# Kernel tuning notes

Hardware: AMD Instinct MI355X
Metric: run time of the kernel (lower is better)

## Reference

```python
import jax, jax.numpy as jnp
import numpy as np
from jax import lax

NL, HID, DIN, DST, DCONV, DTR = 4, 256, 512, 16, 4, 16  # layers, d_model, expand*d_model, d_state, d_conv, dt_rank
B, H, W = 4, 256, 256


def setup_inputs() -> dict:
    key = jax.random.key(0)
    ks = jax.random.split(key, 8)
    def n(k, s, sc=0.02):
        return jax.random.normal(k, s, dtype=jnp.float32) * sc
    return {
        "x": jax.random.normal(ks[0], (B, 3, H, W), dtype=jnp.float32),
        "conv1_w": n(ks[1], (HID // 2, 3, 3, 3), 0.1), "conv1_b": jnp.zeros((HID // 2,), jnp.float32),
        "gn1_w": jnp.ones((HID // 2,), jnp.float32), "gn1_b": jnp.zeros((HID // 2,), jnp.float32),
        "conv2_w": n(ks[2], (HID, HID // 2, 3, 3), 0.05), "conv2_b": jnp.zeros((HID,), jnp.float32),
        "gn2_w": jnp.ones((HID,), jnp.float32), "gn2_b": jnp.zeros((HID,), jnp.float32),
        "ln_w": jnp.ones((NL, HID), jnp.float32), "ln_b": jnp.zeros((NL, HID), jnp.float32),
        "in_proj_w": n(ks[3], (NL, 2 * DIN, HID)),
        "conv1d_w": n(ks[4], (NL, DIN, 1, DCONV), 0.1), "conv1d_b": jnp.zeros((NL, DIN), jnp.float32),
        "x_proj_w": n(ks[5], (NL, DTR + 2 * DST, DIN)),
        "dt_proj_w": n(ks[6], (NL, DIN, DTR), 0.1),
        "dt_proj_b": jnp.full((NL, DIN), -4.6, dtype=jnp.float32),  # softplus(-4.6) ~ 0.01
        "A_log": jnp.broadcast_to(jnp.log(jnp.arange(1, DST + 1, dtype=jnp.float32)), (NL, DIN, DST)) + jnp.zeros((NL, DIN, DST), jnp.float32),
        "D": jnp.ones((NL, DIN), jnp.float32),
        "out_proj_w": n(ks[7], (NL, HID, DIN)),
    }


def conv2d_s2(x, w, b):
    y = lax.conv_general_dilated(x, w, (2, 2), [(1, 1), (1, 1)],
                                 dimension_numbers=('NCHW', 'OIHW', 'NCHW'))
    return y + b[None, :, None, None]


def group_norm(x, w, b, groups=8, eps=1e-5):
    Bb, C, Hh, Ww = x.shape
    xg = x.reshape(Bb, groups, C // groups, Hh, Ww)
    m = xg.mean((2, 3, 4), keepdims=True)
    v = xg.var((2, 3, 4), keepdims=True)
    xg = (xg - m) * lax.rsqrt(v + eps)
    return xg.reshape(Bb, C, Hh, Ww) * w[None, :, None, None] + b[None, :, None, None]


def layer_norm(x, w, b, eps=1e-5):
    m = x.mean(-1, keepdims=True)
    v = x.var(-1, keepdims=True)
    return (x - m) * lax.rsqrt(v + eps) * w + b


def mamba(x, ipw, cw, cb, xpw, dpw, dpb, A_log, Dp, opw):
    # x: [B, L, HID]
    Bb, L, _ = x.shape
    xz = jnp.einsum('bld,ed->ble', x, ipw)           # [B, L, 2*DIN]
    xc, z = jnp.split(xz, 2, axis=-1)
    # depthwise causal conv1d over L
    u = xc.transpose(0, 2, 1)                        # [B, DIN, L]
    u = lax.conv_general_dilated(u, cw, (1,), [(DCONV - 1, 0)],
                                 dimension_numbers=('NCH', 'OIH', 'NCH'),
                                 feature_group_count=DIN)
    xc = jax.nn.silu(u + cb[None, :, None]).transpose(0, 2, 1)  # [B, L, DIN]
    x_dbl = jnp.einsum('bld,ed->ble', xc, xpw)       # [B, L, DTR+2*DST]
    dt, Bm, Cm = jnp.split(x_dbl, [DTR, DTR + DST], axis=-1)
    delta = jax.nn.softplus(jnp.einsum('blr,dr->bld', dt, dpw) + dpb)  # [B, L, DIN]
    A = -jnp.exp(A_log)                              # [DIN, DST]
    dA = jnp.exp(jnp.einsum('bld,dn->bldn', delta, A))
    dBu = jnp.einsum('bld,bln,bld->bldn', delta, Bm, xc)

    def step(h, inp):
        dA_t, dBu_t, C_t = inp
        h = dA_t * h + dBu_t                         # [B, DIN, DST]
        return h, jnp.einsum('bdn,bn->bd', h, C_t)

    h0 = jnp.zeros((Bb, DIN, DST), x.dtype)
    _, ys = lax.scan(step, h0, (dA.transpose(1, 0, 2, 3), dBu.transpose(1, 0, 2, 3), Cm.transpose(1, 0, 2)))
    y = ys.transpose(1, 0, 2) + xc * Dp              # [B, L, DIN]
    y = y * jax.nn.silu(z)
    return jnp.einsum('bld,ed->ble', y, opw)         # [B, L, HID]


def reference(x, conv1_w, conv1_b, gn1_w, gn1_b, conv2_w, conv2_b, gn2_w, gn2_b,
              ln_w, ln_b, in_proj_w, conv1d_w, conv1d_b, x_proj_w, dt_proj_w,
              dt_proj_b, A_log, D, out_proj_w):
    y = jax.nn.silu(group_norm(conv2d_s2(x, conv1_w, conv1_b), gn1_w, gn1_b))
    y = jax.nn.silu(group_norm(conv2d_s2(y, conv2_w, conv2_b), gn2_w, gn2_b))
    Bb, C, h, w = y.shape
    s = y.reshape(Bb, C, h * w).transpose(0, 2, 1)   # b (h w) c
    for i in range(NL):
        s = s + mamba(layer_norm(s, ln_w[i], ln_b[i]), in_proj_w[i], conv1d_w[i],
                      conv1d_b[i], x_proj_w[i], dt_proj_w[i], dt_proj_b[i],
                      A_log[i], D[i], out_proj_w[i])
    return (s, h, w)
```

## Files before the change

### kernel.cpp

```cpp
#include <hip/hip_runtime.h>
#include <math.h>

#define BB 4
#define C1 128
#define H1 128
#define W1 128
#define C2 256
#define H2 64
#define W2 64
#define LSEQ 4096
#define HID 256
#define DIN 512
#define DST 16
#define DTR 16
#define NL 4
#define NCHUNK 64
#define LCH 64

typedef unsigned short u16;
using short8 = __attribute__((ext_vector_type(8))) short;
using f32x4  = __attribute__((ext_vector_type(4))) float;
using f32x2  = __attribute__((ext_vector_type(2))) float;

static __device__ __forceinline__ float dsilu(float x){
    return x / (1.0f + __expf(-x));
}
static __device__ __forceinline__ u16 f2bf(float f){
    unsigned u = __float_as_uint(f);
    u += 0x7FFF + ((u >> 16) & 1);
    return (u16)(u >> 16);
}
static __device__ __forceinline__ float bf2f(u16 v){
    return __uint_as_float(((unsigned)v) << 16);
}

#define GLL16(g, l) __builtin_amdgcn_global_load_lds( \
    (const __attribute__((address_space(1))) void*)(g), \
    (__attribute__((address_space(3))) void*)(l), 16, 0, 0)
#define GLL4(g, l) __builtin_amdgcn_global_load_lds( \
    (const __attribute__((address_space(1))) void*)(g), \
    (__attribute__((address_space(3))) void*)(l), 4, 0, 0)

#define VMW(n) asm volatile("s_waitcnt vmcnt(" #n ")" ::: "memory")

static __device__ __forceinline__ void blockbar(){
    asm volatile("" ::: "memory");
    __builtin_amdgcn_s_barrier();
    asm volatile("" ::: "memory");
}

__global__ void f2bf_kernel(const float* __restrict__ src, u16* __restrict__ dst){
    int idx = blockIdx.x * 256 + threadIdx.x;
    dst[idx] = f2bf(src[idx]);
}
__global__ void wdt_prep_kernel(const float* __restrict__ xpw, const float* __restrict__ dpw,
                                u16* __restrict__ wcomb){
    int idx = blockIdx.x * 256 + threadIdx.x;
    int k = idx & 511;
    int n = (idx >> 9) % 640;
    int layer = idx / (640*512);
    u16 val = 0;
    if(n < 512){
        const float* dp = dpw + ((long)layer*512 + n)*16;
        const float* xp = xpw + (long)layer*48*512 + k;
        float acc = 0.f;
        #pragma unroll
        for(int r = 0; r < 16; ++r) acc = fmaf(dp[r], xp[(long)r*512], acc);
        val = f2bf(acc);
    } else if(n < 544){
        int row = n - 512 + 16;
        val = f2bf(xpw[((long)layer*48 + row)*512 + k]);
    }
    wcomb[((long)layer*640 + n)*512 + k] = val;
}
__global__ void c2w_prep_kernel(const float* __restrict__ src, u16* __restrict__ dst){
    int idx = blockIdx.x * 256 + threadIdx.x;
    int ci = idx & 127, p = (idx >> 7) % 9, co = idx / (9*128);
    int kh = p / 3, kw = p - 3*kh;
    dst[idx] = f2bf(src[((co*128 + ci)*3 + kh)*3 + kw]);
}
__global__ void xt_border_kernel(unsigned* __restrict__ xt){
    int idx = blockIdx.x * 256 + threadIdx.x;
    int c2 = idx & 63;
    int cell = (idx >> 6) % 516;
    int b = idx / (516*64);
    int ih, iw;
    if(cell < 130){ ih = 0; iw = cell; }
    else if(cell < 260){ ih = 129; iw = cell - 130; }
    else if(cell < 388){ iw = 0; ih = cell - 259; }
    else { iw = 129; ih = cell - 387; }
    xt[((long)(b*130 + ih)*130 + iw)*64 + c2] = 0;
}

__global__ __launch_bounds__(256) void conv1_kernel(
        const float* __restrict__ x, const float* __restrict__ w,
        const float* __restrict__ bias, float* __restrict__ y){
    __shared__ float xs[9][260];
    int oh = blockIdx.x, b = blockIdx.y;
    int tid = threadIdx.x;
    #pragma unroll
    for(int r = 0; r < 9; ++r){
        int ci = r / 3, kh = r - 3*ci;
        int ih = 2*oh - 1 + kh;
        float v = 0.f;
        if(ih >= 0) v = x[((b*3 + ci)*256 + ih)*256 + tid];
        xs[r][tid + 1] = v;
        if(tid == 0) xs[r][0] = 0.f;
    }
    __syncthreads();
    int co = tid >> 1, h = tid & 1;
    float wr[27];
    #pragma unroll
    for(int j = 0; j < 27; ++j) wr[j] = w[co*27 + j];
    float bz = bias[co];
    long obase = ((long)((b*128 + co)*128 + oh))*128 + h*64;
    #pragma unroll 4
    for(int i = 0; i < 64; ++i){
        int iw0 = 2*(h*64 + i);
        float acc = bz;
        #pragma unroll
        for(int r = 0; r < 9; ++r){
            acc = fmaf(xs[r][iw0+0], wr[r*3+0], acc);
            acc = fmaf(xs[r][iw0+1], wr[r*3+1], acc);
            acc = fmaf(xs[r][iw0+2], wr[r*3+2], acc);
        }
        y[obase + i] = acc;
    }
}

__global__ void zero_stats_kernel(float* __restrict__ stats){
    stats[threadIdx.x] = 0.0f;
}

__global__ void gn_stats_kernel(const float* __restrict__ x, float* __restrict__ stats,
                                int elems_per_group){
    const int EPB = 16384;
    long base = (long)blockIdx.x * EPB;
    int g = (int)(base / elems_per_group);
    float s = 0.f, ss = 0.f;
    for(int j = threadIdx.x; j < EPB; j += 256){
        float v = x[base + j];
        s += v; ss += v*v;
    }
    #pragma unroll
    for(int off = 32; off; off >>= 1){
        s  += __shfl_down(s,  off);
        ss += __shfl_down(ss, off);
    }
    __shared__ float ls[4], lss[4];
    int wid = threadIdx.x >> 6, lane = threadIdx.x & 63;
    if(lane == 0){ ls[wid] = s; lss[wid] = ss; }
    __syncthreads();
    if(threadIdx.x == 0){
        atomicAdd(&stats[g],      ls[0]+ls[1]+ls[2]+ls[3]);
        atomicAdd(&stats[32+g], lss[0]+lss[1]+lss[2]+lss[3]);
    }
}

__global__ void gn1_transform_kernel(const float* __restrict__ y1, const float* __restrict__ stats,
                                     const float* __restrict__ w, const float* __restrict__ bias,
                                     u16* __restrict__ xt){
    __shared__ float tile[32][33];
    int b = blockIdx.z >> 7, ih = blockIdx.z & 127;
    int c0 = blockIdx.y * 32, w0 = blockIdx.x * 32;
    int tx = threadIdx.x, ty = threadIdx.y;
    const float cnt = 16.f * 128.f * 128.f;
    #pragma unroll
    for(int i = 0; i < 4; ++i){
        int ci = c0 + ty + i*8;
        int g = b*8 + (ci >> 4);
        float mean = stats[g] / cnt;
        float var  = stats[32+g] / cnt - mean*mean;
        float rstd = rsqrtf(var + 1e-5f);
        float v = y1[(((long)(b*C1 + ci))*H1 + ih)*W1 + w0 + tx];
        tile[ty + i*8][tx] = dsilu((v - mean) * rstd * w[ci] + bias[ci]);
    }
    __syncthreads();
    #pragma unroll
    for(int i = 0; i < 4; ++i){
        int iwl = ty + i*8;
        xt[((long)(b*130 + ih + 1)*130 + (w0 + iwl + 1))*128 + c0 + tx] = f2bf(tile[tx][iwl]);
    }
}

__global__ __launch_bounds__(256) void conv2gemm_bf16_kernel(
        const u16* __restrict__ xt, const u16* __restrict__ w2,
        const float* __restrict__ bias, float* __restrict__ y2t){
    __shared__ u16 Asm[3][64*32];
    __shared__ u16 Bsm[3][128*32];
    int m0 = blockIdx.x * 64, n0 = blockIdx.y * 128;
    int tid = threadIdx.x;
    long abase;
    {
        int r = tid >> 2;
        int kq = ((tid & 3) ^ ((r >> 1) & 3)) * 8;
        int m = m0 + r;
        int b = m >> 12, oh = (m >> 6) & 63, ow = m & 63;
        abase = ((long)(b*130 + 2*oh)*130 + 2*ow)*128 + kq;
    }
    int lda = tid*8;
    const u16* bbase[2]; int ldb[2];
    #pragma unroll
    for(int it = 0; it < 2; ++it){
        int c = it*256 + tid;
        int r = c >> 2;
        int kq = ((c & 3) ^ ((r >> 1) & 3)) * 8;
        bbase[it] = w2 + (long)(n0 + r)*1152 + kq;
        ldb[it] = c*8;
    }
    int wave = tid >> 6, lane = tid & 63;
    int wr = wave >> 1, wc = wave & 1;
    int lm = lane & 15, lq = lane >> 4;
    int swq = (lq ^ ((lm >> 1) & 3)) * 8;
    f32x4 acc[2][4] = {};
    #pragma unroll
    for(int pt = 0; pt < 2; ++pt){
        int p = pt >> 2, cs = pt & 3;
        int kh = p / 3, kw = p - 3*kh;
        int ao = (kh*130 + kw)*128 + cs*32;
        GLL16(xt + abase + ao, &Asm[pt][lda]);
        #pragma unroll
        for(int it = 0; it < 2; ++it)
            GLL16(bbase[it] + pt*32, &Bsm[pt][ldb[it]]);
    }
    for(int kk = 0; kk < 36; ++kk){
        int cur = kk % 3;
        if(kk + 2 < 36){
            int k2 = kk + 2;
            int nxt = (kk + 2) % 3;
            int p = k2 >> 2, cs = k2 & 3;
            int kh = p / 3, kw = p - 3*kh;
            int ao = (kh*130 + kw)*128 + cs*32;
            GLL16(xt + abase + ao, &Asm[nxt][lda]);
            #pragma unroll
            for(int it = 0; it < 2; ++it)
                GLL16(bbase[it] + k2*32, &Bsm[nxt][ldb[it]]);
            VMW(6);
        } else if(kk + 1 < 36){
            VMW(3);
        } else {
            VMW(0);
        }
        blockbar();
        short8 af[2], bf[4];
        #pragma unroll
        for(int i = 0; i < 2; ++i)
            af[i] = *(const short8*)&Asm[cur][(wr*32 + i*16 + lm)*32 + swq];
        #pragma unroll
        for(int j = 0; j < 4; ++j)
            bf[j] = *(const short8*)&Bsm[cur][(wc*64 + j*16 + lm)*32 + swq];
        #pragma unroll
        for(int i = 0; i < 2; ++i)
            #pragma unroll
            for(int j = 0; j < 4; ++j)
                acc[i][j] = __builtin_amdgcn_mfma_f32_16x16x32_bf16(af[i], bf[j], acc[i][j], 0, 0, 0);
        __builtin_amdgcn_sched_barrier(0);
        blockbar();
    }
    #pragma unroll
    for(int i = 0; i < 2; ++i){
        long row = m0 + wr*32 + i*16 + lq*4;
        #pragma unroll
        for(int j = 0; j < 4; ++j){
            int col = n0 + wc*64 + j*16 + lm;
            float bz = bias[col];
            #pragma unroll
            for(int r = 0; r < 4; ++r)
                y2t[(row + r)*256L + col] = acc[i][j][r] + bz;
        }
    }
}

__global__ void gn2t_stats_kernel(const float* __restrict__ y2t, float* __restrict__ stats){
    int b = blockIdx.y;
    long row0 = (long)b*LSEQ + blockIdx.x*64;
    int c = threadIdx.x;
    float s = 0.f, ss = 0.f;
    for(int r = 0; r < 64; ++r){
        float v = y2t[(row0 + r)*C2 + c];
        s += v; ss += v*v;
    }
    #pragma unroll
    for(int off = 16; off; off >>= 1){
        s  += __shfl_down(s,  off);
        ss += __shfl_down(ss, off);
    }
    if((c & 31) == 0){
        int g = b*8 + (c >> 5);
        atomicAdd(&stats[g], s);
        atomicAdd(&stats[32+g], ss);
    }
}

__global__ void gn2t_apply_ln_kernel(const float* __restrict__ y2t, const float* __restrict__ stats,
                                     const float* __restrict__ gw, const float* __restrict__ gb,
                                     const float* __restrict__ lw, const float* __restrict__ lb,
                                     float* __restrict__ s, u16* __restrict__ xln){
    long row = blockIdx.x;
    int c = threadIdx.x;
    int b = (int)(row >> 12);
    int g = b*8 + (c >> 5);
    const float cnt = 32.f * (float)LSEQ;
    float mean = stats[g] / cnt;
    float var  = stats[32+g] / cnt - mean*mean;
    float rstd = rsqrtf(var + 1e-5f);
    float v = dsilu((y2t[row*HID + c] - mean) * rstd * gw[c] + gb[c]);
    s[row*HID + c] = v;
    float sm = v, sq = v*v;
    #pragma unroll
    for(int off = 32; off; off >>= 1){
        sm += __shfl_down(sm, off);
        sq += __shfl_down(sq, off);
    }
    __shared__ float pa[4], pb[4], res[2];
    int wid = c >> 6, lane = c & 63;
    if(lane == 0){ pa[wid] = sm; pb[wid] = sq; }
    __syncthreads();
    if(c == 0){
        float t  = pa[0]+pa[1]+pa[2]+pa[3];
        float tt = pb[0]+pb[1]+pb[2]+pb[3];
        float m2 = t / 256.f;
        float v2 = tt / 256.f - m2*m2;
        res[0] = m2; res[1] = rsqrtf(v2 + 1e-5f);
    }
    __syncthreads();
    xln[row*HID + c] = f2bf((v - res[0]) * res[1] * lw[c] + lb[c]);
}

__global__ __launch_bounds__(256) void gemm_bf16_kernel(
        const u16* __restrict__ A, const u16* __restrict__ B, void* __restrict__ Cv,
        int K, int Nact, int ldc, int mode){
    __shared__ u16 Asm[3][128*32];
    __shared__ u16 Bsm[3][128*32];
    int m0 = blockIdx.x * 128, n0 = blockIdx.y * 128;
    int tid = threadIdx.x;
    int wave = tid >> 6, lane = tid & 63;
    int wr = wave >> 1, wc = wave & 1;
    int lm = lane & 15, lq = lane >> 4;
    int swq = (lq ^ ((lm >> 1) & 3)) * 8;
    const u16* ag[2]; const u16* bg[2]; int ldst[2];
    #pragma unroll
    for(int it = 0; it < 2; ++it){
        int c = it*256 + tid;
        int r = c >> 2;
        int kq = ((c & 3) ^ ((r >> 1) & 3)) * 8;
        ag[it] = A + (long)(m0 + r)*K + kq;
        bg[it] = B + (long)(n0 + r)*K + kq;
        ldst[it] = c*8;
    }
    f32x4 acc[4][4] = {};
    int nk = K >> 5;
    #pragma unroll
    for(int pt = 0; pt < 2; ++pt){
        int ko = pt << 5;
        #pragma unroll
        for(int it = 0; it < 2; ++it){
            GLL16(ag[it] + ko, &Asm[pt][ldst[it]]);
            GLL16(bg[it] + ko, &Bsm[pt][ldst[it]]);
        }
    }
    for(int kt = 0; kt < nk; ++kt){
        int cur = kt % 3;
        if(kt + 2 < nk){
            int nxt = (kt + 2) % 3;
            int ko = (kt + 2) << 5;
            #pragma unroll
            for(int it = 0; it < 2; ++it){
                GLL16(ag[it] + ko, &Asm[nxt][ldst[it]]);
                GLL16(bg[it] + ko, &Bsm[nxt][ldst[it]]);
            }
            VMW(8);
        } else if(kt + 1 < nk){
            VMW(4);
        } else {
            VMW(0);
        }
        blockbar();
        short8 af[4], bf[4];
        #pragma unroll
        for(int i = 0; i < 4; ++i){
            af[i] = *(const short8*)&Asm[cur][(wr*64 + i*16 + lm)*32 + swq];
            bf[i] = *(const short8*)&Bsm[cur][(wc*64 + i*16 + lm)*32 + swq];
        }
        #pragma unroll
        for(int i = 0; i < 4; ++i)
            #pragma unroll
            for(int j = 0; j < 4; ++j)
                acc[i][j] = __builtin_amdgcn_mfma_f32_16x16x32_bf16(af[i], bf[j], acc[i][j], 0, 0, 0);
        __builtin_amdgcn_sched_barrier(0);
        blockbar();
    }
    #pragma unroll
    for(int i = 0; i < 4; ++i){
        long row = m0 + wr*64 + i*16 + lq*4;
        #pragma unroll
        for(int j = 0; j < 4; ++j){
            int col = n0 + wc*64 + j*16 + lm;
            if(col < Nact){
                #pragma unroll
                for(int r = 0; r < 4; ++r){
                    long idx = (row + r)*(long)ldc + col;
                    if(mode == 2) ((u16*)Cv)[idx] = f2bf(acc[i][j][r]);
                    else          ((float*)Cv)[idx] = acc[i][j][r];
                }
            }
        }
    }
}

__global__ __launch_bounds__(256) void gemm_dtbc_kernel(
        const u16* __restrict__ A, const u16* __restrict__ B,
        const float* __restrict__ dpb, u16* __restrict__ dv,
        float* __restrict__ xdbl32){
    __shared__ u16 Asm[3][128*32];
    __shared__ u16 Bsm[3][128*32];
    int m0 = blockIdx.x * 128, n0 = blockIdx.y * 128;
    int tid = threadIdx.x;
    int wave = tid >> 6, lane = tid & 63;
    int wr = wave >> 1, wc = wave & 1;
    int lm = lane & 15, lq = lane >> 4;
    int swq = (lq ^ ((lm >> 1) & 3)) * 8;
    const u16* ag[2]; const u16* bg[2]; int ldst[2];
    #pragma unroll
    for(int it = 0; it < 2; ++it){
        int c = it*256 + tid;
        int r = c >> 2;
        int kq = ((c & 3) ^ ((r >> 1) & 3)) * 8;
        ag[it] = A + (long)(m0 + r)*512 + kq;
        bg[it] = B + (long)(n0 + r)*512 + kq;
        ldst[it] = c*8;
    }
    f32x4 acc[4][4] = {};
    #pragma unroll
    for(int pt = 0; pt < 2; ++pt){
        int ko = pt << 5;
        #pragma unroll
        for(int it = 0; it < 2; ++it){
            GLL16(ag[it] + ko, &Asm[pt][ldst[it]]);
            GLL16(bg[it] + ko, &Bsm[pt][ldst[it]]);
        }
    }
    for(int kt = 0; kt < 16; ++kt){
        int cur = kt % 3;
        if(kt + 2 < 16){
            int nxt = (kt + 2) % 3;
            int ko = (kt + 2) << 5;
            #pragma unroll
            for(int it = 0; it < 2; ++it){
                GLL16(ag[it] + ko, &Asm[nxt][ldst[it]]);
                GLL16(bg[it] + ko, &Bsm[nxt][ldst[it]]);
            }
            VMW(8);
        } else if(kt + 1 < 16){
            VMW(4);
        } else {
            VMW(0);
        }
        blockbar();
        short8 af[4], bf[4];
        #pragma unroll
        for(int i = 0; i < 4; ++i){
            af[i] = *(const short8*)&Asm[cur][(wr*64 + i*16 + lm)*32 + swq];
            bf[i] = *(const short8*)&Bsm[cur][(wc*64 + i*16 + lm)*32 + swq];
        }
        #pragma unroll
        for(int i = 0; i < 4; ++i)
            #pragma unroll
            for(int j = 0; j < 4; ++j)
                acc[i][j] = __builtin_amdgcn_mfma_f32_16x16x32_bf16(af[i], bf[j], acc[i][j], 0, 0, 0);
        __builtin_amdgcn_sched_barrier(0);
        blockbar();
    }
    if(n0 < 512){
        #pragma unroll
        for(int i = 0; i < 4; ++i){
            long row = m0 + wr*64 + i*16 + lq*4;
            #pragma unroll
            for(int j = 0; j < 4; ++j){
                int col = n0 + wc*64 + j*16 + lm;
                float bz = dpb[col];
                #pragma unroll
                for(int r = 0; r < 4; ++r){
                    float v = acc[i][j][r] + bz;
                    v = (v > 20.f) ? v : __logf(1.f + __expf(v));
                    dv[(row + r)*512L + col] = f2bf(v);
                }
            }
        }
    } else {
        #pragma unroll
        for(int i = 0; i < 4; ++i){
            long row = m0 + wr*64 + i*16 + lq*4;
            #pragma unroll
            for(int j = 0; j < 4; ++j){
                int lcol = wc*64 + j*16 + lm;
                if(lcol < 32){
                    #pragma unroll
                    for(int r = 0; r < 4; ++r)
                        xdbl32[(row + r)*32L + lcol] = acc[i][j][r];
                }
            }
        }
    }
}

__global__ __launch_bounds__(256) void gemm_out_ln_kernel(
        const u16* __restrict__ A, const u16* __restrict__ B,
        float* __restrict__ s, u16* __restrict__ xln,
        const float* __restrict__ lw, const float* __restrict__ lb){
    __shared__ u16 Asm[3][32*32];
    __shared__ u16 Bsm[3][256*32];
    __shared__ float lnred[2][2][16][2];
    int m0 = blockIdx.x * 32;
    int tid = threadIdx.x;
    int wave = tid >> 6, lane = tid & 63;
    int wr = wave >> 1, wc = wave & 1;
    int lm = lane & 15, lq = lane >> 4;
    int swq = (lq ^ ((lm >> 1) & 3)) * 8;
    const u16* agA[2]; int lda[2];
    #pragma unroll
    for(int it = 0; it < 2; ++it){
        int c = it*256 + tid;
        int r = c >> 4;
        int kp = (c & 15) * 2;
        int kel = ((((c & 15) >> 2) ^ ((r >> 1) & 3)) << 3) + (kp & 7);
        agA[it] = A + (long)(m0 + r)*512 + kel;
        lda[it] = c*2;
    }
    const u16* bg[4]; int ldb[4];
    #pragma unroll
    for(int it = 0; it < 4; ++it){
        int c = it*256 + tid;
        int r = c >> 2;
        int kq = ((c & 3) ^ ((r >> 1) & 3)) * 8;
        bg[it] = B + (long)r*512 + kq;
        ldb[it] = c*8;
    }
    f32x4 acc[8] = {};
    #pragma unroll
    for(int pt = 0; pt < 2; ++pt){
        int ko = pt << 5;
        #pragma unroll
        for(int it = 0; it < 2; ++it) GLL4(agA[it] + ko, &Asm[pt][lda[it]]);
        #pragma unroll
        for(int it = 0; it < 4; ++it) GLL16(bg[it] + ko, &Bsm[pt][ldb[it]]);
    }
    for(int kt = 0; kt < 16; ++kt){
        int cur = kt % 3;
        if(kt + 2 < 16){
            int nxt = (kt + 2) % 3;
            int ko = (kt + 2) << 5;
            #pragma unroll
            for(int it = 0; it < 2; ++it) GLL4(agA[it] + ko, &Asm[nxt][lda[it]]);
            #pragma unroll
            for(int it = 0; it < 4; ++it) GLL16(bg[it] + ko, &Bsm[nxt][ldb[it]]);
            VMW(12);
        } else if(kt + 1 < 16){
            VMW(6);
        } else {
            VMW(0);
        }
        blockbar();
        short8 af = *(const short8*)&Asm[cur][(wr*16 + lm)*32 + swq];
        #pragma unroll
        for(int j = 0; j < 8; ++j){
            short8 bf = *(const short8*)&Bsm[cur][(wc*128 + j*16 + lm)*32 + swq];
            acc[j] = __builtin_amdgcn_mfma_f32_16x16x32_bf16(af, bf, acc[j], 0, 0, 0);
        }
        __builtin_amdgcn_sched_barrier(0);
        blockbar();
    }
    int row0 = m0 + wr*16 + lq*4;
    float psum[4] = {0.f,0.f,0.f,0.f}, psq[4] = {0.f,0.f,0.f,0.f};
    #pragma unroll
    for(int j = 0; j < 8; ++j){
        int col = wc*128 + j*16 + lm;
        #pragma unroll
        for(int r = 0; r < 4; ++r){
            long idx = (long)(row0 + r)*HID + col;
            float v = s[idx] + acc[j][r];
            acc[j][r] = v;
            s[idx] = v;
            psum[r] += v; psq[r] += v*v;
        }
    }
    #pragma unroll
    for(int mask = 1; mask <= 8; mask <<= 1){
        #pragma unroll
        for(int r = 0; r < 4; ++r){
            psum[r] += __shfl_xor(psum[r], mask);
            psq[r]  += __shfl_xor(psq[r],  mask);
        }
    }
    if(lm == 0){
        #pragma unroll
        for(int r = 0; r < 4; ++r){
            lnred[wr][wc][lq*4 + r][0] = psum[r];
            lnred[wr][wc][lq*4 + r][1] = psq[r];
        }
    }
    __syncthreads();
    float mean[4], rstd[4];
    #pragma unroll
    for(int r = 0; r < 4; ++r){
        float t  = lnred[wr][0][lq*4 + r][0] + lnred[wr][1][lq*4 + r][0];
        float tt = lnred[wr][0][lq*4 + r][1] + lnred[wr][1][lq*4 + r][1];
        mean[r] = t * (1.f/256.f);
        float var = tt * (1.f/256.f) - mean[r]*mean[r];
        rstd[r] = rsqrtf(var + 1e-5f);
    }
    #pragma unroll
    for(int j = 0; j < 8; ++j){
        int col = wc*128 + j*16 + lm;
        float wv = lw[col], bv = lb[col];
        #pragma unroll
        for(int r = 0; r < 4; ++r){
            long idx = (long)(row0 + r)*HID + col;
            xln[idx] = f2bf((acc[j][r] - mean[r]) * rstd[r] * wv + bv);
        }
    }
}

__global__ void conv1d_silu_kernel(const u16* __restrict__ xz, const float* __restrict__ w,
                                   const float* __restrict__ bias, u16* __restrict__ xcv){
    int idx = blockIdx.x * 256 + threadIdx.x;
    int e = idx * 8;
    int d0 = e & 511;
    long m = e >> 9;
    int l = (int)(m & 4095);
    short8 xrow[4];
    const u16* xp = xz + m*(2*DIN) + d0;
    #pragma unroll
    for(int j = 0; j < 4; ++j){
        int t = l - 3 + j;
        if(t >= 0) xrow[j] = *(const short8*)(xp + (long)(j-3)*(2*DIN));
        else       xrow[j] = (short8){0,0,0,0,0,0,0,0};
    }
    float wv[8][4];
    #pragma unroll
    for(int k = 0; k < 8; k += 2){
        float4 a = *(const float4*)(w + (d0+k)*4);
        float4 b = *(const float4*)(w + (d0+k+1)*4);
        wv[k][0]=a.x; wv[k][1]=a.y; wv[k][2]=a.z; wv[k][3]=a.w;
        wv[k+1][0]=b.x; wv[k+1][1]=b.y; wv[k+1][2]=b.z; wv[k+1][3]=b.w;
    }
    float bz[8];
    {
        float4 a = *(const float4*)(bias + d0);
        float4 b = *(const float4*)(bias + d0 + 4);
        bz[0]=a.x; bz[1]=a.y; bz[2]=a.z; bz[3]=a.w;
        bz[4]=b.x; bz[5]=b.y; bz[6]=b.z; bz[7]=b.w;
    }
    short8 out;
    #pragma unroll
    for(int k = 0; k < 8; ++k){
        float acc = bz[k];
        #pragma unroll
        for(int j = 0; j < 4; ++j)
            acc = fmaf(bf2f((u16)xrow[j][k]), wv[k][j], acc);
        out[k] = (short)f2bf(dsilu(acc));
    }
    *(short8*)(xcv + m*DIN + d0) = out;
}

__global__ __launch_bounds__(256) void scan1_kernel(
        const u16* __restrict__ xcvb, const u16* __restrict__ dvin,
        const float* __restrict__ xdbl32, const float* __restrict__ Alog,
        float* __restrict__ aprod, float* __restrict__ hend){
    int d = blockIdx.y * 256 + threadIdx.x;
    int c = blockIdx.x;
    int b = blockIdx.z;
    __shared__ float bm[LCH][16];
    {
        int t = threadIdx.x >> 4, n = threadIdx.x & 15;
        #pragma unroll
        for(int it = 0; it < 4; ++it){
            long p = ((long)(b*LSEQ + c*LCH + t + it*16))*32;
            bm[t + it*16][n] = xdbl32[p + n];
        }
    }
    __syncthreads();
    float An[16];
    #pragma unroll
    for(int n = 0; n < 16; ++n)
        An[n] = -__expf(Alog[d*16 + n]);
    float An0 = An[0];
    bool structural = true;
    #pragma unroll
    for(int n = 0; n < 16; ++n)
        structural = structural && (fabsf(An[n] - (float)(n+1)*An0) <= 1e-3f*(float)(n+1));
    long base = ((long)(b*LSEQ + c*LCH))*DIN + d;
    long ob = (((long)(b*NCHUNK + c))*DIN + d)*16;
    if(structural){
        f32x2 h2[8];
        #pragma unroll
        for(int i = 0; i < 8; ++i) h2[i] = (f32x2){0.f, 0.f};
        float sumdv = 0.f;
        float xv_n = bf2f(xcvb[base]);
        float dv_n = bf2f(dvin[base]);
        for(int t = 0; t < LCH; ++t){
            float xv = xv_n, dv = dv_n;
            if(t + 1 < LCH){
                xv_n = bf2f(xcvb[base + (long)(t+1)*DIN]);
                dv_n = bf2f(dvin[base + (long)(t+1)*DIN]);
            }
            sumdv += dv;
            float db = dv * xv;
            float r1 = __expf(dv * An0);
            float r2 = r1 * r1;
            f32x2 rr = {r2, r2};
            f32x2 e2[8];
            e2[0] = (f32x2){r1, r2};
            #pragma unroll
            for(int i = 1; i < 8; ++i) e2[i] = e2[i-1] * rr;
            f32x2 db2 = {db, db};
            const f32x2* b2 = (const f32x2*)&bm[t][0];
            #pragma unroll
            for(int i = 0; i < 8; ++i) h2[i] = e2[i]*h2[i] + db2*b2[i];
        }
        float R = __expf(An0 * sumdv);
        float Rp = R;
        const float* hp = (const float*)h2;
        #pragma unroll
        for(int n = 0; n < 16; ++n){
            aprod[ob+n] = Rp; Rp *= R;
            hend[ob+n] = hp[n];
        }
    } else {
        float h[16], ap[16];
        #pragma unroll
        for(int n = 0; n < 16; ++n){ h[n] = 0.f; ap[n] = 1.f; }
        for(int t = 0; t < LCH; ++t){
            float dv = bf2f(dvin[base + (long)t*DIN]);
            float db = dv * bf2f(xcvb[base + (long)t*DIN]);
            #pragma unroll
            for(int n = 0; n < 16; ++n){
                float e = __expf(dv * An[n]);
                ap[n] *= e;
                h[n] = fmaf(e, h[n], db * bm[t][n]);
            }
        }
        #pragma unroll
        for(int n = 0; n < 16; ++n){ aprod[ob+n] = ap[n]; hend[ob+n] = h[n]; }
    }
}

__global__ void scan2_kernel(const float* __restrict__ aprod, const float* __restrict__ hend,
                             float* __restrict__ hinit){
    int idx = blockIdx.x * 256 + threadIdx.x;
    int n = idx & 15, d = (idx >> 4) & 511, b = idx >> 13;
    const long stride = (long)DIN * 16;
    long p0 = (((long)(b*NCHUNK))*DIN + d)*16 + n;
    float h = 0.f;
    for(int c = 0; c < NCHUNK; c += 8){
        float a[8], e[8];
        #pragma unroll
        for(int j = 0; j < 8; ++j){
            long p = p0 + (long)(c + j)*stride;
            a[j] = aprod[p]; e[j] = hend[p];
        }
        #pragma unroll
        for(int j = 0; j < 8; ++j){
            hinit[p0 + (long)(c + j)*stride] = h;
            h = fmaf(a[j], h, e[j]);
        }
    }
}

__global__ __launch_bounds__(256) void scan3_kernel(
        const u16* __restrict__ xcvb, const u16* __restrict__ dvin,
        const float* __restrict__ xdbl32, const float* __restrict__ Alog,
        const float* __restrict__ hinit, const float* __restrict__ Dp,
        const u16* __restrict__ xz, u16* __restrict__ yout){
    int d = blockIdx.y * 256 + threadIdx.x;
    int c = blockIdx.x;
    int b = blockIdx.z;
    __shared__ float bm[LCH][16], cm[LCH][16];
    {
        int t = threadIdx.x >> 4, n = threadIdx.x & 15;
        #pragma unroll
        for(int it = 0; it < 4; ++it){
            long p = ((long)(b*LSEQ + c*LCH + t + it*16))*32;
            bm[t + it*16][n] = xdbl32[p + n];
            cm[t + it*16][n] = xdbl32[p + 16 + n];
        }
    }
    __syncthreads();
    float An[16];
    long hb = (((long)(b*NCHUNK + c))*DIN + d)*16;
    #pragma unroll
    for(int n = 0; n < 16; ++n)
        An[n] = -__expf(Alog[d*16 + n]);
    float An0 = An[0];
    bool structural = true;
    #pragma unroll
    for(int n = 0; n < 16; ++n)
        structural = structural && (fabsf(An[n] - (float)(n+1)*An0) <= 1e-3f*(float)(n+1));
    float Dv = Dp[d];
    long base  = ((long)(b*LSEQ + c*LCH))*DIN + d;
    long zbase = ((long)(b*LSEQ + c*LCH))*(2*DIN) + DIN + d;
    if(structural){
        f32x2 h2[8];
        {
            const f32x2* hi = (const f32x2*)&hinit[hb];
            #pragma unroll
            for(int i = 0; i < 8; ++i) h2[i] = hi[i];
        }
        float xv_n = bf2f(xcvb[base]);
        float z_n  = bf2f(xz[zbase]);
        float dv_n = bf2f(dvin[base]);
        for(int t = 0; t < LCH; ++t){
            float xv = xv_n, z = z_n, dv = dv_n;
            if(t + 1 < LCH){
                xv_n = bf2f(xcvb[base + (long)(t+1)*DIN]);
                z_n  = bf2f(xz[zbase + (long)(t+1)*(2*DIN)]);
                dv_n = bf2f(dvin[base + (long)(t+1)*DIN]);
            }
            float db = dv * xv;
            float r1 = __expf(dv * An0);
            float r2 = r1 * r1;
            f32x2 rr = {r2, r2};
            f32x2 e2[8];
            e2[0] = (f32x2){r1, r2};
            #pragma unroll
            for(int i = 1; i < 8; ++i) e2[i] = e2[i-1] * rr;
            f32x2 db2 = {db, db};
            const f32x2* b2 = (const f32x2*)&bm[t][0];
            const f32x2* c2 = (const f32x2*)&cm[t][0];
            f32x2 y2 = {0.f, 0.f};
            #pragma unroll
            for(int i = 0; i < 8; ++i){
                h2[i] = e2[i]*h2[i] + db2*b2[i];
                y2 = y2 + h2[i]*c2[i];
            }
            float y = y2[0] + y2[1];
            y = fmaf(xv, Dv, y);
            yout[base + (long)t*DIN] = f2bf(y * dsilu(z));
        }
    } else {
        float h[16];
        #pragma unroll
        for(int n = 0; n < 16; ++n) h[n] = hinit[hb + n];
        for(int t = 0; t < LCH; ++t){
            float dv = bf2f(dvin[base + (long)t*DIN]);
            float xv = bf2f(xcvb[base + (long)t*DIN]);
            float db = dv * xv;
            float y = 0.f;
            #pragma unroll
            for(int n = 0; n < 16; ++n){
                float e = __expf(dv * An[n]);
                h[n] = fmaf(e, h[n], db * bm[t][n]);
                y = fmaf(h[n], cm[t][n], y);
            }
            y = fmaf(xv, Dv, y);
            float z = bf2f(xz[zbase + (long)t*(2*DIN)]);
            yout[base + (long)t*DIN] = f2bf(y * dsilu(z));
        }
    }
}

__global__ void copyout_kernel(const float* __restrict__ s, float* __restrict__ out, int out_size){
    int idx = blockIdx.x * 256 + threadIdx.x;
    if(idx >= out_size) return;
    out[idx] = (idx < BB*LSEQ*HID) ? s[idx] : 64.0f;
}

extern "C" void kernel_launch(void* const* d_in, const int* in_sizes, int n_in,
                              void* d_out, int out_size, void* d_ws, size_t ws_size,
                              hipStream_t stream){
    const float* x        = (const float*)d_in[0];
    const float* conv1_w  = (const float*)d_in[1];
    const float* conv1_b  = (const float*)d_in[2];
    const float* gn1_w    = (const float*)d_in[3];
    const float* gn1_b    = (const float*)d_in[4];
    const float* conv2_w  = (const float*)d_in[5];
    const float* conv2_b  = (const float*)d_in[6];
    const float* gn2_w    = (const float*)d_in[7];
    const float* gn2_b    = (const float*)d_in[8];
    const float* ln_w     = (const float*)d_in[9];
    const float* ln_b     = (const float*)d_in[10];
    const float* in_proj  = (const float*)d_in[11];
    const float* c1d_w    = (const float*)d_in[12];
    const float* c1d_b    = (const float*)d_in[13];
    const float* x_proj   = (const float*)d_in[14];
    const float* dt_w     = (const float*)d_in[15];
    const float* dt_b     = (const float*)d_in[16];
    const float* A_log    = (const float*)d_in[17];
    const float* Dvec     = (const float*)d_in[18];
    const float* out_proj = (const float*)d_in[19];

    float* ws = (float*)d_ws;
    float* s      = ws;
    u16*   xz_bf  = (u16*)(ws + 4194304);
    float* y1     = ws + 4194304;
    u16*   xt     = (u16*)(ws + 12582912);
    u16*   xcv_bf = (u16*)(ws + 16909312);
    float* y2t    = ws + 16909312;
    u16*   xln_bf = (u16*)(ws + 21103616);
    float* xdbl   = ws + 23200768;
    float* aprod  = ws + 23987200;
    float* hendb  = ws + 28181504;
    u16*   y_bf   = (u16*)aprod;
    float* hinit  = ws + 32375808;
    float* stats  = ws + 36570112;
    u16*   ipw_bf = (u16*)(ws + 36570176);
    u16*   opw_bf = ipw_bf + 1048576;
    u16*   c2w_bf = opw_bf + 524288;
    u16*   dv_bf  = (u16*)(ws + 37635200);
    u16*   wcomb  = (u16*)(ws + 41829504);

    f2bf_kernel<<<4096, 256, 0, stream>>>(in_proj, ipw_bf);
    f2bf_kernel<<<2048, 256, 0, stream>>>(out_proj, opw_bf);
    c2w_prep_kernel<<<1152, 256, 0, stream>>>(conv2_w, c2w_bf);
    wdt_prep_kernel<<<5120, 256, 0, stream>>>(x_proj, dt_w, wcomb);

    conv1_kernel<<<dim3(128,4), 256, 0, stream>>>(x, conv1_w, conv1_b, y1);
    zero_stats_kernel<<<1, 64, 0, stream>>>(stats);
    gn_stats_kernel<<<512, 256, 0, stream>>>(y1, stats, 16*H1*W1);
    xt_border_kernel<<<516, 256, 0, stream>>>((unsigned*)xt);
    gn1_transform_kernel<<<dim3(4,4,512), dim3(32,8), 0, stream>>>(y1, stats, gn1_w, gn1_b, xt);
    conv2gemm_bf16_kernel<<<dim3(256,2), 256, 0, stream>>>(xt, c2w_bf, conv2_b, y2t);
    zero_stats_kernel<<<1, 64, 0, stream>>>(stats);
    gn2t_stats_kernel<<<dim3(64,4), 256, 0, stream>>>(y2t, stats);
    gn2t_apply_ln_kernel<<<16384, 256, 0, stream>>>(y2t, stats, gn2_w, gn2_b,
                                                    ln_w, ln_b, s, xln_bf);

    for(int layer = 0; layer < NL; ++layer){
        const float* cw  = c1d_w + (long)layer*DIN*4;
        const float* cb  = c1d_b + (long)layer*DIN;
        const float* dpb = dt_b  + (long)layer*DIN;
        const float* Al  = A_log + (long)layer*DIN*DST;
        const float* Dl  = Dvec  + (long)layer*DIN;
        int lnext = (layer + 1) & 3;

        gemm_bf16_kernel<<<dim3(128,8), 256, 0, stream>>>(
            xln_bf, ipw_bf + (long)layer*1024*256, xz_bf, HID, 2*DIN, 2*DIN, 2);
        conv1d_silu_kernel<<<4096, 256, 0, stream>>>(xz_bf, cw, cb, xcv_bf);
        gemm_dtbc_kernel<<<dim3(128,5), 256, 0, stream>>>(
            xcv_bf, wcomb + (long)layer*640*512, dpb, dv_bf, xdbl);
        scan1_kernel<<<dim3(NCHUNK,2,BB), 256, 0, stream>>>(
            xcv_bf, dv_bf, xdbl, Al, aprod, hendb);
        scan2_kernel<<<128, 256, 0, stream>>>(aprod, hendb, hinit);
        scan3_kernel<<<dim3(NCHUNK,2,BB), 256, 0, stream>>>(
            xcv_bf, dv_bf, xdbl, Al, hinit, Dl, xz_bf, y_bf);
        gemm_out_ln_kernel<<<512, 256, 0, stream>>>(
            y_bf, opw_bf + (long)layer*256*512, s, xln_bf,
            ln_w + lnext*HID, ln_b + lnext*HID);
    }

    copyout_kernel<<<(out_size + 255)/256, 256, 0, stream>>>(s, (float*)d_out, out_size);
}
```

Measured before the change: 783.7 us.

## Fuse three scan phases into one kernel with grid barriers

Merges the chunked scan's three kernels (per-chunk reduction, cross-chunk prefix, output pass) into one persistent kernel that uses atomic grid barriers between phases. The xconv chunk stays in shared memory across phases, so it is loaded once instead of twice, and B/C are staged up front. It also skips MFMA work in the dt/B/C GEMM for the partially used last N tile. The risks are deadlock if all 512 blocks are not co-resident, plus barrier spin overhead.

```diff
diff --git a/kernel.cpp b/kernel.cpp
--- a/kernel.cpp
+++ b/kernel.cpp
@@ -49,6 +49,17 @@
     asm volatile("" ::: "memory");
 }
 
+static __device__ __forceinline__ void gridbar(unsigned* bar, unsigned target){
+    __threadfence();
+    __syncthreads();
+    if(threadIdx.x == 0){
+        atomicAdd(bar, 1u);
+        while(atomicAdd(bar, 0u) < target){ __builtin_amdgcn_s_sleep(2); }
+    }
+    __syncthreads();
+    __threadfence();
+}
+
 __global__ void f2bf_kernel(const float* __restrict__ src, u16* __restrict__ dst){
     int idx = blockIdx.x * 256 + threadIdx.x;
     dst[idx] = f2bf(src[idx]);
@@ -90,6 +101,9 @@
     else if(cell < 388){ iw = 0; ih = cell - 259; }
     else { iw = 129; ih = cell - 387; }
     xt[((long)(b*130 + ih)*130 + iw)*64 + c2] = 0;
+}
+__global__ void bar_init_kernel(unsigned* __restrict__ bar){
+    bar[threadIdx.x] = 0;
 }
 
 __global__ __launch_bounds__(256) void conv1_kernel(
@@ -420,6 +434,7 @@
     int wr = wave >> 1, wc = wave & 1;
     int lm = lane & 15, lq = lane >> 4;
     int swq = (lq ^ ((lm >> 1) & 3)) * 8;
+    int jlim = (n0 < 512) ? 4 : ((wc == 0) ? 2 : 0);
     const u16* ag[2]; const u16* bg[2]; int ldst[2];
     #pragma unroll
     for(int it = 0; it < 2; ++it){
@@ -457,17 +472,16 @@
             VMW(0);
         }
         blockbar();
-        short8 af[4], bf[4];
-        #pragma unroll
-        for(int i = 0; i < 4; ++i){
+        short8 af[4];
+        #pragma unroll
+        for(int i = 0; i < 4; ++i)
             af[i] = *(const short8*)&Asm[cur][(wr*64 + i*16 + lm)*32 + swq];
-            bf[i] = *(const short8*)&Bsm[cur][(wc*64 + i*16 + lm)*32 + swq];
-        }
-        #pragma unroll
-        for(int i = 0; i < 4; ++i)
-            #pragma unroll
-            for(int j = 0; j < 4; ++j)
-                acc[i][j] = __builtin_amdgcn_mfma_f32_16x16x32_bf16(af[i], bf[j], acc[i][j], 0, 0, 0);
+        for(int j = 0; j < jlim; ++j){
+            short8 bf = *(const short8*)&Bsm[cur][(wc*64 + j*16 + lm)*32 + swq];
+            #pragma unroll
+            for(int i = 0; i < 4; ++i)
+                acc[i][j] = __builtin_amdgcn_mfma_f32_16x16x32_bf16(af[i], bf, acc[i][j], 0, 0, 0);
+        }
         __builtin_amdgcn_sched_barrier(0);
         blockbar();
     }
@@ -663,23 +677,37 @@
     *(short8*)(xcv + m*DIN + d0) = out;
 }
 
-__global__ __launch_bounds__(256) void scan1_kernel(
+__global__ __launch_bounds__(256, 2) void scan_fused_kernel(
         const u16* __restrict__ xcvb, const u16* __restrict__ dvin,
         const float* __restrict__ xdbl32, const float* __restrict__ Alog,
-        float* __restrict__ aprod, float* __restrict__ hend){
-    int d = blockIdx.y * 256 + threadIdx.x;
-    int c = blockIdx.x;
-    int b = blockIdx.z;
-    __shared__ float bm[LCH][16];
+        const float* __restrict__ Dp, const u16* __restrict__ xz,
+        float* __restrict__ aprod, float* __restrict__ hend,
+        float* __restrict__ hinit, u16* __restrict__ yout,
+        unsigned* __restrict__ bar){
+    __shared__ u16 xls[LCH*256];
+    __shared__ float bm[LCH][16], cm[LCH][16];
+    int tid = threadIdx.x;
+    int c = blockIdx.x, dh = blockIdx.y, b = blockIdx.z;
+    int d = dh*256 + tid;
     {
-        int t = threadIdx.x >> 4, n = threadIdx.x & 15;
+        int t = tid >> 4, n = tid & 15;
         #pragma unroll
         for(int it = 0; it < 4; ++it){
             long p = ((long)(b*LSEQ + c*LCH + t + it*16))*32;
             bm[t + it*16][n] = xdbl32[p + n];
-        }
-    }
+            cm[t + it*16][n] = xdbl32[p + 16 + n];
+        }
+    }
+    #pragma unroll
+    for(int it = 0; it < 8; ++it){
+        int e = it*256 + tid;
+        int tt = e >> 5, q = e & 31;
+        long g = ((long)(b*LSEQ + c*LCH + tt))*DIN + dh*256 + q*8;
+        GLL16(xcvb + g, &xls[e*8]);
+    }
+    VMW(0);
     __syncthreads();
+
     float An[16];
     #pragma unroll
     for(int n = 0; n < 16; ++n)
@@ -691,19 +719,17 @@
         structural = structural && (fabsf(An[n] - (float)(n+1)*An0) <= 1e-3f*(float)(n+1));
     long base = ((long)(b*LSEQ + c*LCH))*DIN + d;
     long ob = (((long)(b*NCHUNK + c))*DIN + d)*16;
+
     if(structural){
         f32x2 h2[8];
         #pragma unroll
         for(int i = 0; i < 8; ++i) h2[i] = (f32x2){0.f, 0.f};
         float sumdv = 0.f;
-        float xv_n = bf2f(xcvb[base]);
         float dv_n = bf2f(dvin[base]);
         for(int t = 0; t < LCH; ++t){
-            float xv = xv_n, dv = dv_n;
-            if(t + 1 < LCH){
-                xv_n = bf2f(xcvb[base + (long)(t+1)*DIN]);
-                dv_n = bf2f(dvin[base + (long)(t+1)*DIN]);
-            }
+            float dv = dv_n;
+            if(t + 1 < LCH) dv_n = bf2f(dvin[base + (long)(t+1)*DIN]);
+            float xv = bf2f(xls[t*256 + tid]);
             sumdv += dv;
             float db = dv * xv;
             float r1 = __expf(dv * An0);
@@ -732,7 +758,7 @@
         for(int n = 0; n < 16; ++n){ h[n] = 0.f; ap[n] = 1.f; }
         for(int t = 0; t < LCH; ++t){
             float dv = bf2f(dvin[base + (long)t*DIN]);
-            float db = dv * bf2f(xcvb[base + (long)t*DIN]);
+            float db = dv * bf2f(xls[t*256 + tid]);
             #pragma unroll
             for(int n = 0; n < 16; ++n){
                 float e = __expf(dv * An[n]);
@@ -743,61 +769,37 @@
         #pragma unroll
         for(int n = 0; n < 16; ++n){ aprod[ob+n] = ap[n]; hend[ob+n] = h[n]; }
     }
-}
-
-__global__ void scan2_kernel(const float* __restrict__ aprod, const float* __restrict__ hend,
-                             float* __restrict__ hinit){
-    int idx = blockIdx.x * 256 + threadIdx.x;
-    int n = idx & 15, d = (idx >> 4) & 511, b = idx >> 13;
-    const long stride = (long)DIN * 16;
-    long p0 = (((long)(b*NCHUNK))*DIN + d)*16 + n;
-    float h = 0.f;
-    for(int c = 0; c < NCHUNK; c += 8){
-        float a[8], e[8];
-        #pragma unroll
-        for(int j = 0; j < 8; ++j){
-            long p = p0 + (long)(c + j)*stride;
-            a[j] = aprod[p]; e[j] = hend[p];
-        }
-        #pragma unroll
-        for(int j = 0; j < 8; ++j){
-            hinit[p0 + (long)(c + j)*stride] = h;
-            h = fmaf(a[j], h, e[j]);
-        }
-    }
-}
-
-__global__ __launch_bounds__(256) void scan3_kernel(
-        const u16* __restrict__ xcvb, const u16* __restrict__ dvin,
-        const float* __restrict__ xdbl32, const float* __restrict__ Alog,
-        const float* __restrict__ hinit, const float* __restrict__ Dp,
-        const u16* __restrict__ xz, u16* __restrict__ yout){
-    int d = blockIdx.y * 256 + threadIdx.x;
-    int c = blockIdx.x;
-    int b = blockIdx.z;
-    __shared__ float bm[LCH][16], cm[LCH][16];
+
+    gridbar(bar + 0, 512);
+
     {
-        int t = threadIdx.x >> 4, n = threadIdx.x & 15;
-        #pragma unroll
-        for(int it = 0; it < 4; ++it){
-            long p = ((long)(b*LSEQ + c*LCH + t + it*16))*32;
-            bm[t + it*16][n] = xdbl32[p + n];
-            cm[t + it*16][n] = xdbl32[p + 16 + n];
-        }
-    }
-    __syncthreads();
-    float An[16];
-    long hb = (((long)(b*NCHUNK + c))*DIN + d)*16;
-    #pragma unroll
-    for(int n = 0; n < 16; ++n)
-        An[n] = -__expf(Alog[d*16 + n]);
-    float An0 = An[0];
-    bool structural = true;
-    #pragma unroll
-    for(int n = 0; n < 16; ++n)
-        structural = structural && (fabsf(An[n] - (float)(n+1)*An0) <= 1e-3f*(float)(n+1));
+        int bid = (b*2 + dh)*NCHUNK + c;
+        int gtid = bid*256 + tid;
+        if(gtid < 32768){
+            int n2 = gtid & 15, d2 = (gtid >> 4) & 511, b2 = gtid >> 13;
+            const long stride = (long)DIN * 16;
+            long p0 = (((long)(b2*NCHUNK))*DIN + d2)*16 + n2;
+            float h = 0.f;
+            for(int cc = 0; cc < NCHUNK; cc += 8){
+                float a[8], e[8];
+                #pragma unroll
+                for(int j = 0; j < 8; ++j){
+                    long p = p0 + (long)(cc + j)*stride;
+                    a[j] = aprod[p]; e[j] = hend[p];
+                }
+                #pragma unroll
+                for(int j = 0; j < 8; ++j){
+                    hinit[p0 + (long)(cc + j)*stride] = h;
+                    h = fmaf(a[j], h, e[j]);
+                }
+            }
+        }
+    }
+
+    gridbar(bar + 1, 512);
+
+    long hb = ob;
     float Dv = Dp[d];
-    long base  = ((long)(b*LSEQ + c*LCH))*DIN + d;
     long zbase = ((long)(b*LSEQ + c*LCH))*(2*DIN) + DIN + d;
     if(structural){
         f32x2 h2[8];
@@ -806,16 +808,15 @@
             #pragma unroll
             for(int i = 0; i < 8; ++i) h2[i] = hi[i];
         }
-        float xv_n = bf2f(xcvb[base]);
         float z_n  = bf2f(xz[zbase]);
         float dv_n = bf2f(dvin[base]);
         for(int t = 0; t < LCH; ++t){
-            float xv = xv_n, z = z_n, dv = dv_n;
+            float z = z_n, dv = dv_n;
             if(t + 1 < LCH){
-                xv_n = bf2f(xcvb[base + (long)(t+1)*DIN]);
                 z_n  = bf2f(xz[zbase + (long)(t+1)*(2*DIN)]);
                 dv_n = bf2f(dvin[base + (long)(t+1)*DIN]);
             }
+            float xv = bf2f(xls[t*256 + tid]);
             float db = dv * xv;
             float r1 = __expf(dv * An0);
             float r2 = r1 * r1;
@@ -843,7 +844,7 @@
         for(int n = 0; n < 16; ++n) h[n] = hinit[hb + n];
         for(int t = 0; t < LCH; ++t){
             float dv = bf2f(dvin[base + (long)t*DIN]);
-            float xv = bf2f(xcvb[base + (long)t*DIN]);
+            float xv = bf2f(xls[t*256 + tid]);
             float db = dv * xv;
             float y = 0.f;
             #pragma unroll
@@ -898,6 +899,7 @@
     float* y2t    = ws + 16909312;
     u16*   xln_bf = (u16*)(ws + 21103616);
     float* xdbl   = ws + 23200768;
+    unsigned* bars = (unsigned*)(ws + 23725056);
     float* aprod  = ws + 23987200;
     float* hendb  = ws + 28181504;
     u16*   y_bf   = (u16*)aprod;
@@ -909,6 +911,7 @@
     u16*   dv_bf  = (u16*)(ws + 37635200);
     u16*   wcomb  = (u16*)(ws + 41829504);
 
+    bar_init_kernel<<<1, 16, 0, stream>>>(bars);
     f2bf_kernel<<<4096, 256, 0, stream>>>(in_proj, ipw_bf);
     f2bf_kernel<<<2048, 256, 0, stream>>>(out_proj, opw_bf);
     c2w_prep_kernel<<<1152, 256, 0, stream>>>(conv2_w, c2w_bf);
@@ -938,11 +941,9 @@
         conv1d_silu_kernel<<<4096, 256, 0, stream>>>(xz_bf, cw, cb, xcv_bf);
         gemm_dtbc_kernel<<<dim3(128,5), 256, 0, stream>>>(
             xcv_bf, wcomb + (long)layer*640*512, dpb, dv_bf, xdbl);
-        scan1_kernel<<<dim3(NCHUNK,2,BB), 256, 0, stream>>>(
-            xcv_bf, dv_bf, xdbl, Al, aprod, hendb);
-        scan2_kernel<<<128, 256, 0, stream>>>(aprod, hendb, hinit);
-        scan3_kernel<<<dim3(NCHUNK,2,BB), 256, 0, stream>>>(
-            xcv_bf, dv_bf, xdbl, Al, hinit, Dl, xz_bf, y_bf);
+        scan_fused_kernel<<<dim3(NCHUNK,2,BB), 256, 0, stream>>>(
+            xcv_bf, dv_bf, xdbl, Al, Dl, xz_bf, aprod, hendb, hinit, y_bf,
+            bars + layer*2);
         gemm_out_ln_kernel<<<512, 256, 0, stream>>>(
             y_bf, opw_bf + (long)layer*256*512, s, xln_bf,
             ln_w + lnext*HID, ln_b + lnext*HID);
```

Measured after the change: 2.376 ms. +203.2%, slower.
